# Optimization experiments

Hardware: AMD Instinct MI355X
Metric: run time of the kernel (lower is better)

The kernel has to match this reference:

```python
import jax, jax.numpy as jnp
import numpy as np

B, C = 16384, 4096

def setup_inputs() -> dict:
    key = jax.random.key(0)
    k1, k2 = jax.random.split(key)
    output = jax.random.normal(k1, (B, C), dtype=jnp.float32)
    target = jax.random.randint(k2, (B, C), 0, 2, dtype=jnp.int32)  # multi-hot 0/1
    return {"output": output, "target": target}

def reference(output, target):
    # softmax over class dim (dim=1 in torch)
    p = jax.nn.softmax(output, axis=1)  # [B, C]
    # loss[b] = log(sum_n exp(p[b,n])) - sum_{n: target[b,n]==1} p[b,n]
    lse = jax.scipy.special.logsumexp(p, axis=1)              # [B]
    masked = jnp.sum(p * (target == 1).astype(p.dtype), axis=1)  # [B]
    loss = lse - masked
    return jnp.mean(loss)
```

## Files before the change

### kernel.cpp

```cpp
#include <hip/hip_runtime.h>

constexpr int C_CLS = 4096;
constexpr int BLOCK = 256;
constexpr int WAVES = BLOCK / 64;
constexpr int VEC_ITERS = C_CLS / (BLOCK * 4);

typedef float v4f __attribute__((ext_vector_type(4)));
typedef int v4i __attribute__((ext_vector_type(4)));

__device__ inline float wave_reduce_sum(float v) {
#pragma unroll
    for (int off = 32; off > 0; off >>= 1) v += __shfl_down(v, off, 64);
    return v;
}

template <bool ATOMIC>
__global__ __launch_bounds__(BLOCK) void ce_row_kernel(const float* __restrict__ x,
                                                       const int* __restrict__ tgt,
                                                       float* __restrict__ dst,
                                                       float inv_b) {
    const int b = blockIdx.x;
    const int tid = threadIdx.x;
    const int lane = tid & 63;
    const int wave = tid >> 6;

    const v4f* xr = reinterpret_cast<const v4f*>(x + (size_t)b * C_CLS);
    const v4i* tr = reinterpret_cast<const v4i*>(tgt + (size_t)b * C_CLS);

    v4f xv[VEC_ITERS];
    v4i tv[VEC_ITERS];
#pragma unroll
    for (int i = 0; i < VEC_ITERS; ++i) {
        xv[i] = __builtin_nontemporal_load(&xr[tid + i * BLOCK]);
        tv[i] = __builtin_nontemporal_load(&tr[tid + i * BLOCK]);
    }

    float s1 = 0.f, s2 = 0.f, s3 = 0.f, sm = 0.f;
#pragma unroll
    for (int i = 0; i < VEC_ITERS; ++i) {
        const float e0 = __expf(xv[i].x);
        const float e1 = __expf(xv[i].y);
        const float e2 = __expf(xv[i].z);
        const float e3 = __expf(xv[i].w);
        s1 += (e0 + e1) + (e2 + e3);
        const float q0 = e0 * e0, q1 = e1 * e1, q2 = e2 * e2, q3 = e3 * e3;
        s2 += (q0 + q1) + (q2 + q3);
        s3 += (q0 * e0 + q1 * e1) + (q2 * e2 + q3 * e3);
        sm += (tv[i].x == 1 ? e0 : 0.f) + (tv[i].y == 1 ? e1 : 0.f) +
              (tv[i].z == 1 ? e2 : 0.f) + (tv[i].w == 1 ? e3 : 0.f);
    }

    s1 = wave_reduce_sum(s1);
    s2 = wave_reduce_sum(s2);
    s3 = wave_reduce_sum(s3);
    sm = wave_reduce_sum(sm);

    __shared__ float sh[4][WAVES];
    if (lane == 0) {
        sh[0][wave] = s1; sh[1][wave] = s2; sh[2][wave] = s3; sh[3][wave] = sm;
    }
    __syncthreads();
    if (tid == 0) {
        const float S1 = (sh[0][0] + sh[0][1]) + (sh[0][2] + sh[0][3]);
        const float S2 = (sh[1][0] + sh[1][1]) + (sh[1][2] + sh[1][3]);
        const float S3 = (sh[2][0] + sh[2][1]) + (sh[2][2] + sh[2][3]);
        const float Sm = (sh[3][0] + sh[3][1]) + (sh[3][2] + sh[3][3]);
        const float inv = 1.f / S1;
        const float sum_exp_p = (float)C_CLS + 1.f +
                                inv * inv * (0.5f * S2 + 0.16666667f * inv * S3);
        const float loss = __logf(sum_exp_p) - Sm * inv;
        if (ATOMIC) {
            atomicAdd(dst, loss * inv_b);
        } else {
            dst[b] = loss;
        }
    }
}

__global__ __launch_bounds__(BLOCK) void ce_reduce_kernel(const float* __restrict__ rl,
                                                          float* __restrict__ out,
                                                          int n4, float inv_b) {
    const v4f* r4 = reinterpret_cast<const v4f*>(rl);
    float s = 0.f;
    for (int i = threadIdx.x; i < n4; i += BLOCK) {
        const v4f v = r4[i];
        s += (v.x + v.y) + (v.z + v.w);
    }
    s = wave_reduce_sum(s);
    __shared__ float sh[WAVES];
    const int lane = threadIdx.x & 63;
    const int wave = threadIdx.x >> 6;
    if (lane == 0) sh[wave] = s;
    __syncthreads();
    if (threadIdx.x == 0) out[0] = ((sh[0] + sh[1]) + (sh[2] + sh[3])) * inv_b;
}

__global__ void ce_zero_kernel(float* out) { out[0] = 0.f; }

extern "C" void kernel_launch(void* const* d_in, const int* in_sizes, int n_in,
                              void* d_out, int out_size, void* d_ws, size_t ws_size,
                              hipStream_t stream) {
    const float* x = (const float*)d_in[0];
    const int* tgt = (const int*)d_in[1];
    float* out = (float*)d_out;

    const int B = in_sizes[0] / C_CLS;
    const float inv_b = 1.0f / (float)B;

    if (ws_size >= (size_t)B * sizeof(float)) {
        float* row_loss = (float*)d_ws;
        ce_row_kernel<false><<<B, BLOCK, 0, stream>>>(x, tgt, row_loss, inv_b);
        ce_reduce_kernel<<<1, BLOCK, 0, stream>>>(row_loss, out, B / 4, inv_b);
    } else {
        ce_zero_kernel<<<1, 1, 0, stream>>>(out);
        ce_row_kernel<true><<<B, BLOCK, 0, stream>>>(x, tgt, out, inv_b);
    }
}
```

Baseline: 473.3 us.

## Map one row per wavefront with chunked streaming loads instead of one row per block

Each 64-lane wavefront now handles a whole row, looping over it in chunks of four vec4 loads. This removes the shared-memory cross-wave reduction and the block barrier, and cuts the grid by a factor of four. The mask select is replaced by an int-to-float multiply. The cost is fewer bytes in flight per wave, since the unroll-1 loop issues only 8 vec4 loads at a time instead of the whole row up front. That could reduce memory-level parallelism for this bandwidth-bound kernel.

New measurement: 473.6 us. No clear change (+0.1%).

```diff
diff --git a/kernel.cpp b/kernel.cpp
--- a/kernel.cpp
+++ b/kernel.cpp
@@ -3,7 +3,8 @@
 constexpr int C_CLS = 4096;
 constexpr int BLOCK = 256;
 constexpr int WAVES = BLOCK / 64;
-constexpr int VEC_ITERS = C_CLS / (BLOCK * 4);
+constexpr int LANE_V4 = C_CLS / (64 * 4);
+constexpr int CHUNK = 4;
 
 typedef float v4f __attribute__((ext_vector_type(4)));
 typedef int v4i __attribute__((ext_vector_type(4)));
@@ -18,36 +19,39 @@
 __global__ __launch_bounds__(BLOCK) void ce_row_kernel(const float* __restrict__ x,
                                                        const int* __restrict__ tgt,
                                                        float* __restrict__ dst,
-                                                       float inv_b) {
-    const int b = blockIdx.x;
-    const int tid = threadIdx.x;
-    const int lane = tid & 63;
-    const int wave = tid >> 6;
+                                                       float inv_b, int nrows) {
+    const int lane = threadIdx.x & 63;
+    const int wave = threadIdx.x >> 6;
+    const int row = blockIdx.x * WAVES + wave;
+    if (row >= nrows) return;
 
-    const v4f* xr = reinterpret_cast<const v4f*>(x + (size_t)b * C_CLS);
-    const v4i* tr = reinterpret_cast<const v4i*>(tgt + (size_t)b * C_CLS);
-
-    v4f xv[VEC_ITERS];
-    v4i tv[VEC_ITERS];
-#pragma unroll
-    for (int i = 0; i < VEC_ITERS; ++i) {
-        xv[i] = __builtin_nontemporal_load(&xr[tid + i * BLOCK]);
-        tv[i] = __builtin_nontemporal_load(&tr[tid + i * BLOCK]);
-    }
+    const v4f* xr = reinterpret_cast<const v4f*>(x + (size_t)row * C_CLS);
+    const v4i* tr = reinterpret_cast<const v4i*>(tgt + (size_t)row * C_CLS);
 
     float s1 = 0.f, s2 = 0.f, s3 = 0.f, sm = 0.f;
+#pragma unroll 1
+    for (int c = 0; c < LANE_V4; c += CHUNK) {
+        v4f xv[CHUNK];
+        v4i tv[CHUNK];
 #pragma unroll
-    for (int i = 0; i < VEC_ITERS; ++i) {
-        const float e0 = __expf(xv[i].x);
-        const float e1 = __expf(xv[i].y);
-        const float e2 = __expf(xv[i].z);
-        const float e3 = __expf(xv[i].w);
-        s1 += (e0 + e1) + (e2 + e3);
-        const float q0 = e0 * e0, q1 = e1 * e1, q2 = e2 * e2, q3 = e3 * e3;
-        s2 += (q0 + q1) + (q2 + q3);
-        s3 += (q0 * e0 + q1 * e1) + (q2 * e2 + q3 * e3);
-        sm += (tv[i].x == 1 ? e0 : 0.f) + (tv[i].y == 1 ? e1 : 0.f) +
-              (tv[i].z == 1 ? e2 : 0.f) + (tv[i].w == 1 ? e3 : 0.f);
+        for (int i = 0; i < CHUNK; ++i)
+            xv[i] = __builtin_nontemporal_load(&xr[lane + (c + i) * 64]);
+#pragma unroll
+        for (int i = 0; i < CHUNK; ++i)
+            tv[i] = __builtin_nontemporal_load(&tr[lane + (c + i) * 64]);
+#pragma unroll
+        for (int i = 0; i < CHUNK; ++i) {
+            const float e0 = __expf(xv[i].x);
+            const float e1 = __expf(xv[i].y);
+            const float e2 = __expf(xv[i].z);
+            const float e3 = __expf(xv[i].w);
+            s1 += (e0 + e1) + (e2 + e3);
+            const float q0 = e0 * e0, q1 = e1 * e1, q2 = e2 * e2, q3 = e3 * e3;
+            s2 += (q0 + q1) + (q2 + q3);
+            s3 += (q0 * e0 + q1 * e1) + (q2 * e2 + q3 * e3);
+            sm += (float)tv[i].x * e0 + (float)tv[i].y * e1 +
+                  (float)tv[i].z * e2 + (float)tv[i].w * e3;
+        }
     }
 
     s1 = wave_reduce_sum(s1);
@@ -55,24 +59,15 @@
     s3 = wave_reduce_sum(s3);
     sm = wave_reduce_sum(sm);
 
-    __shared__ float sh[4][WAVES];
     if (lane == 0) {
-        sh[0][wave] = s1; sh[1][wave] = s2; sh[2][wave] = s3; sh[3][wave] = sm;
-    }
-    __syncthreads();
-    if (tid == 0) {
-        const float S1 = (sh[0][0] + sh[0][1]) + (sh[0][2] + sh[0][3]);
-        const float S2 = (sh[1][0] + sh[1][1]) + (sh[1][2] + sh[1][3]);
-        const float S3 = (sh[2][0] + sh[2][1]) + (sh[2][2] + sh[2][3]);
-        const float Sm = (sh[3][0] + sh[3][1]) + (sh[3][2] + sh[3][3]);
-        const float inv = 1.f / S1;
+        const float inv = 1.f / s1;
         const float sum_exp_p = (float)C_CLS + 1.f +
-                                inv * inv * (0.5f * S2 + 0.16666667f * inv * S3);
-        const float loss = __logf(sum_exp_p) - Sm * inv;
+                                inv * inv * (0.5f * s2 + 0.16666667f * inv * s3);
+        const float loss = __logf(sum_exp_p) - sm * inv;
         if (ATOMIC) {
             atomicAdd(dst, loss * inv_b);
         } else {
-            dst[b] = loss;
+            dst[row] = loss;
         }
     }
 }
@@ -106,13 +101,14 @@
 
     const int B = in_sizes[0] / C_CLS;
     const float inv_b = 1.0f / (float)B;
+    const int grid = (B + WAVES - 1) / WAVES;
 
     if (ws_size >= (size_t)B * sizeof(float)) {
         float* row_loss = (float*)d_ws;
-        ce_row_kernel<false><<<B, BLOCK, 0, stream>>>(x, tgt, row_loss, inv_b);
+        ce_row_kernel<false><<<grid, BLOCK, 0, stream>>>(x, tgt, row_loss, inv_b, B);
         ce_reduce_kernel<<<1, BLOCK, 0, stream>>>(row_loss, out, B / 4, inv_b);
     } else {
         ce_zero_kernel<<<1, 1, 0, stream>>>(out);
-        ce_row_kernel<true><<<B, BLOCK, 0, stream>>>(x, tgt, out, inv_b);
+        ce_row_kernel<true><<<grid, BLOCK, 0, stream>>>(x, tgt, out, inv_b, B);
     }
 }
```
